# Kernel optimization log

Hardware: AMD Instinct MI355X
Metric: run time of the kernel (lower is better)

## Reference

```python
import jax, jax.numpy as jnp
import numpy as np


def setup_inputs() -> dict:
    key = jax.random.key(0)
    k1, k2, k3, k4, k5 = jax.random.split(key, 5)
    B, D_IN, D_OUT = 8192, 4096, 4096
    inp = jax.random.normal(k1, (B, D_IN), dtype=jnp.float32)
    # dir_loc: kaiming-like init then row-normalized (as in __init__)
    dir_loc = jax.random.normal(k2, (D_OUT, D_IN), dtype=jnp.float32) * np.sqrt(2.0 / D_IN)
    dir_loc = dir_loc / jnp.sqrt(jnp.sum(dir_loc ** 2, axis=-1, keepdims=True))
    # raw (softplus-inverse) concentration parameter
    dir_conc_raw = jax.random.uniform(k3, (D_OUT,), dtype=jnp.float32) + 3.0
    # rad_layer = nn.Linear(in, out): default torch init ~ U(-1/sqrt(in), 1/sqrt(in))
    bound = 1.0 / np.sqrt(D_IN)
    rad_w = jax.random.uniform(k4, (D_OUT, D_IN), minval=-bound, maxval=bound, dtype=jnp.float32)
    rad_b = jax.random.uniform(k5, (D_OUT,), minval=-bound, maxval=bound, dtype=jnp.float32)
    bias = jnp.zeros((D_OUT,), dtype=jnp.float32)  # initialized uniform(0,0)
    return {"input": inp, "dir_loc": dir_loc, "dir_conc_raw": dir_conc_raw,
            "rad_w": rad_w, "rad_b": rad_b, "bias": bias}


def reference(input, dir_loc, dir_conc_raw, rad_w, rad_b, bias):
    # sample=False path: direction_sample = PowerSpherical(loc, kappa).mean
    #   = loc * kappa / (kappa + dim - 1), kappa = softplus(raw)
    d = dir_loc.shape[1]
    kappa = jax.nn.softplus(dir_conc_raw)                      # [O]
    direction = dir_loc * (kappa / (kappa + (d - 1)))[:, None]  # [O, I]
    # radius = softplus(Linear(input))
    radius = jax.nn.softplus(input @ rad_w.T + rad_b)          # [B, O]
    # (input.unsqueeze(1) * (direction * radius[..., None])).sum(-1) + bias
    # == (input @ direction.T) * radius + bias  (GEMM + elementwise scale)
    return (input @ direction.T) * radius + bias
```

## Files before the change

kernel.cpp:

```cpp
#include <hip/hip_runtime.h>
#include <hip/hip_bf16.h>
#include <math.h>


typedef __bf16 bf16x8 __attribute__((ext_vector_type(8)));
typedef float  f32x4  __attribute__((ext_vector_type(4)));
typedef unsigned short u16;
typedef u16   u16x4 __attribute__((ext_vector_type(4)));
typedef float f4    __attribute__((ext_vector_type(4)));

#define BDIM 8192
#define IDIM 4096
#define ODIM 4096
#define BM 256
#define BN 128
#define BK 32
#define NKT (IDIM/BK)

__device__ __forceinline__ u16 f2bf(float x){ __bf16 h=(__bf16)x; return __builtin_bit_cast(u16,h); }
__device__ __forceinline__ float bf2f(u16 u){ return (float)__builtin_bit_cast(__bf16,u); }

__global__ void k_scale(const float* __restrict__ raw, float* __restrict__ scale){
  int o = blockIdx.x*256 + threadIdx.x;
  if(o < ODIM){
    float x = raw[o];
    float k = (x > 20.f) ? x : log1pf(expf(x));
    scale[o] = k / (k + (float)(IDIM-1));
  }
}

__global__ void k_split(const f4* __restrict__ src, u16x4* __restrict__ hi,
                        u16x4* __restrict__ lo, int n4){
  int i = blockIdx.x*blockDim.x + threadIdx.x;
  int stride = gridDim.x*blockDim.x;
  for(; i<n4; i+=stride){
    f4 v = src[i];
    u16x4 h, l;
    #pragma unroll
    for(int j=0;j<4;++j){
      float x = v[j];
      u16 hb = f2bf(x);
      h[j] = hb;
      l[j] = f2bf(x - bf2f(hb));
    }
    hi[i]=h; lo[i]=l;
  }
}

__global__ void k_split_dir(const f4* __restrict__ src, const float* __restrict__ scale,
                            u16x4* __restrict__ hi, u16x4* __restrict__ lo, int n4){
  int i = blockIdx.x*blockDim.x + threadIdx.x;
  int stride = gridDim.x*blockDim.x;
  for(; i<n4; i+=stride){
    float s = scale[i>>10];
    f4 v = src[i];
    u16x4 h, l;
    #pragma unroll
    for(int j=0;j<4;++j){
      float x = v[j]*s;
      u16 hb = f2bf(x);
      h[j] = hb;
      l[j] = f2bf(x - bf2f(hb));
    }
    hi[i]=h; lo[i]=l;
  }
}

__device__ __forceinline__ void async16(const u16* g, u16* l){
  __builtin_amdgcn_global_load_lds((const __attribute__((address_space(1))) void*)g,
                                   (__attribute__((address_space(3))) void*)l, 16, 0, 0);
}

__global__ __launch_bounds__(512,2) void k_gemm(
    const u16* __restrict__ Ah, const u16* __restrict__ Al,
    const u16* __restrict__ Rh, const u16* __restrict__ Rl,
    const u16* __restrict__ Dh, const u16* __restrict__ Dl,
    const float* __restrict__ rad_b, const float* __restrict__ bias,
    float* __restrict__ out)
{
  __shared__ __align__(16) u16 smem[2*32768];

  const int tid  = threadIdx.x;
  const int lane = tid & 63;
  const int wid  = tid >> 6;
  const int wr = wid >> 1, wc = wid & 1;

  const int bid = blockIdx.x;
  const int swz = (bid & 7)*128 + (bid >> 3);
  const int bm = swz >> 5;
  const int bn = swz & 31;

  const int r0   = tid >> 2;
  const int cxor = (r0 >> 1) & 3;
  const int c0   = ((tid & 3) ^ cxor) * 8;
  const size_t arow = (size_t)(bm*BM + r0)*IDIM + c0;
  const size_t brow = (size_t)(bn*BN + r0)*IDIM + c0;
  const u16* gAh = Ah + arow;  const u16* gAl = Al + arow;
  const u16* gRh = Rh + brow;  const u16* gRl = Rl + brow;
  const u16* gDh = Dh + brow;  const u16* gDl = Dl + brow;
  u16* dst = smem + tid*8;

  const int lr   = lane & 15;
  const int koff = (((lane >> 4) ^ ((lr >> 1) & 3))) * 8;
  const int aoff = (wr*64 + lr)*BK + koff;
  const int boff = (wc*64 + lr)*BK + koff;

  f32x4 accR[4][4] = {};
  f32x4 accD[4][4] = {};

#define MFMA16(A,B,C) __builtin_amdgcn_mfma_f32_16x16x32_bf16(A,B,C,0,0,0)

#define STAGE_FULL(BUF, KT) { \
    const int _k = (KT)*BK; \
    u16* _df = dst + (BUF)*32768; \
    async16(gAh + _k,            _df);         \
    async16(gAh + 128*IDIM + _k, _df + 4096);  \
    async16(gAl + _k,            _df + 8192);  \
    async16(gAl + 128*IDIM + _k, _df + 12288); \
    async16(gRh + _k,            _df + 16384); \
    async16(gRl + _k,            _df + 20480); \
    async16(gDh + _k,            _df + 24576); \
    async16(gDl + _k,            _df + 28672); \
  }

#define PH_PRE  __builtin_amdgcn_s_barrier(); \
    asm volatile("s_waitcnt lgkmcnt(0)" ::: "memory"); \
    __builtin_amdgcn_sched_barrier(0); \
    __builtin_amdgcn_s_setprio(1);
#define PH_POST __builtin_amdgcn_s_setprio(0); \
    __builtin_amdgcn_s_barrier(); \
    __builtin_amdgcn_sched_barrier(0);

#define K_TILE(BUF, VM, DOSTAGE, NEXTK) { \
    const u16* sb = smem + (BUF)*32768; \
    const int _ko = (NEXTK)*BK; \
    u16* _d = dst + (BUF)*32768; \
    bf16x8 ah[4], al[4]; \
    {  \
      bf16x8 b0[2], b1[2]; \
      _Pragma("unroll") for(int mi=0;mi<4;++mi){ \
        ah[mi] = *(const bf16x8*)(sb +        aoff + mi*512); \
        al[mi] = *(const bf16x8*)(sb + 8192 + aoff + mi*512); } \
      _Pragma("unroll") for(int ni=0;ni<2;++ni){ \
        b0[ni] = *(const bf16x8*)(sb + 16384 + boff + ni*512); \
        b1[ni] = *(const bf16x8*)(sb + 20480 + boff + ni*512); } \
      PH_PRE \
      _Pragma("unroll") for(int mi=0;mi<4;++mi) \
        _Pragma("unroll") for(int ni=0;ni<2;++ni){ \
          accR[mi][ni] = MFMA16(ah[mi], b0[ni], accR[mi][ni]); \
          accR[mi][ni] = MFMA16(ah[mi], b1[ni], accR[mi][ni]); \
          accR[mi][ni] = MFMA16(al[mi], b0[ni], accR[mi][ni]); } \
      PH_POST \
    } \
    {  \
      bf16x8 b0[2], b1[2]; \
      _Pragma("unroll") for(int ni=0;ni<2;++ni){ \
        b0[ni] = *(const bf16x8*)(sb + 16384 + boff + (ni+2)*512); \
        b1[ni] = *(const bf16x8*)(sb + 20480 + boff + (ni+2)*512); } \
      if (DOSTAGE) { \
        async16(gAh + _ko,            _d);         \
        async16(gAh + 128*IDIM + _ko, _d + 4096);  \
        async16(gAl + _ko,            _d + 8192);  \
        async16(gAl + 128*IDIM + _ko, _d + 12288); } \
      PH_PRE \
      _Pragma("unroll") for(int mi=0;mi<4;++mi) \
        _Pragma("unroll") for(int ni=0;ni<2;++ni){ \
          accR[mi][ni+2] = MFMA16(ah[mi], b0[ni], accR[mi][ni+2]); \
          accR[mi][ni+2] = MFMA16(ah[mi], b1[ni], accR[mi][ni+2]); \
          accR[mi][ni+2] = MFMA16(al[mi], b0[ni], accR[mi][ni+2]); } \
      PH_POST \
    } \
    {  \
      bf16x8 b0[2], b1[2]; \
      _Pragma("unroll") for(int ni=0;ni<2;++ni){ \
        b0[ni] = *(const bf16x8*)(sb + 24576 + boff + ni*512); \
        b1[ni] = *(const bf16x8*)(sb + 28672 + boff + ni*512); } \
      if (DOSTAGE) { \
        async16(gRh + _ko, _d + 16384); \
        async16(gRl + _ko, _d + 20480); } \
      PH_PRE \
      _Pragma("unroll") for(int mi=0;mi<4;++mi) \
        _Pragma("unroll") for(int ni=0;ni<2;++ni){ \
          accD[mi][ni] = MFMA16(ah[mi], b0[ni], accD[mi][ni]); \
          accD[mi][ni] = MFMA16(ah[mi], b1[ni], accD[mi][ni]); \
          accD[mi][ni] = MFMA16(al[mi], b0[ni], accD[mi][ni]); } \
      PH_POST \
    } \
    {  \
      bf16x8 b0[2], b1[2]; \
      _Pragma("unroll") for(int ni=0;ni<2;++ni){ \
        b0[ni] = *(const bf16x8*)(sb + 24576 + boff + (ni+2)*512); \
        b1[ni] = *(const bf16x8*)(sb + 28672 + boff + (ni+2)*512); } \
      PH_PRE \
      _Pragma("unroll") for(int mi=0;mi<4;++mi) \
        _Pragma("unroll") for(int ni=0;ni<2;++ni){ \
          accD[mi][ni+2] = MFMA16(ah[mi], b0[ni], accD[mi][ni+2]); \
          accD[mi][ni+2] = MFMA16(ah[mi], b1[ni], accD[mi][ni+2]); \
          accD[mi][ni+2] = MFMA16(al[mi], b0[ni], accD[mi][ni+2]); } \
      __builtin_amdgcn_s_setprio(0); \
      asm volatile("s_waitcnt vmcnt(" VM ")" ::: "memory"); \
      __builtin_amdgcn_s_barrier(); \
      __builtin_amdgcn_sched_barrier(0); \
      if (DOSTAGE) { \
        async16(gDh + _ko, _d + 24576); \
        async16(gDl + _ko, _d + 28672); } \
    } \
  }

  STAGE_FULL(0, 0)
  STAGE_FULL(1, 1)
  asm volatile("s_waitcnt vmcnt(8)" ::: "memory");
  __builtin_amdgcn_s_barrier();
  __builtin_amdgcn_sched_barrier(0);

  #pragma unroll 1
  for(int t=0; t<NKT-2; t+=2){
    K_TILE(0, "6", true, t+2)
    K_TILE(1, "6", true, t+3)
  }
  K_TILE(0, "0", false, 0)
  K_TILE(1, "0", false, 0)

#undef K_TILE
#undef PH_PRE
#undef PH_POST
#undef STAGE_FULL
#undef MFMA16

  const int orow0 = bm*BM + wr*64 + (lane>>4)*4;
  const int ocol0 = bn*BN + wc*64 + (lane & 15);
  #pragma unroll
  for(int ni=0;ni<4;++ni){
    const int col = ocol0 + ni*16;
    const float rb = rad_b[col];
    const float bs = bias[col];
    #pragma unroll
    for(int mi=0;mi<4;++mi){
      const int row = orow0 + mi*16;
      #pragma unroll
      for(int j=0;j<4;++j){
        float s  = accR[mi][ni][j] + rb;
        float sp = (s > 20.f) ? s : log1pf(expf(s));
        out[(size_t)(row+j)*ODIM + col] = accD[mi][ni][j]*sp + bs;
      }
    }
  }
}

extern "C" void kernel_launch(void* const* d_in, const int* in_sizes, int n_in,
                              void* d_out, int out_size, void* d_ws, size_t ws_size,
                              hipStream_t stream){
  (void)in_sizes; (void)n_in; (void)out_size; (void)ws_size;
  const float* inp  = (const float*)d_in[0];
  const float* dirl = (const float*)d_in[1];
  const float* draw = (const float*)d_in[2];
  const float* radw = (const float*)d_in[3];
  const float* radb = (const float*)d_in[4];
  const float* bias = (const float*)d_in[5];
  float* out = (float*)d_out;

  char* ws = (char*)d_ws;
  u16* Ah = (u16*)(ws);
  u16* Al = (u16*)(ws +  67108864L);
  u16* Rh = (u16*)(ws + 134217728L);
  u16* Rl = (u16*)(ws + 167772160L);
  u16* Dh = (u16*)(ws + 201326592L);
  u16* Dl = (u16*)(ws + 234881024L);
  float* scale = (float*)(ws + 268435456L);

  k_scale<<<dim3(ODIM/256), dim3(256), 0, stream>>>(draw, scale);

  const int n4A = BDIM*IDIM/4;
  const int n4W = ODIM*IDIM/4;
  k_split<<<dim3(2048), dim3(256), 0, stream>>>((const f4*)inp,  (u16x4*)Ah, (u16x4*)Al, n4A);
  k_split<<<dim3(2048), dim3(256), 0, stream>>>((const f4*)radw, (u16x4*)Rh, (u16x4*)Rl, n4W);
  k_split_dir<<<dim3(2048), dim3(256), 0, stream>>>((const f4*)dirl, scale, (u16x4*)Dh, (u16x4*)Dl, n4W);

  k_gemm<<<dim3((BDIM/BM)*(ODIM/BN)), dim3(512), 0, stream>>>(
      Ah, Al, Rh, Rl, Dh, Dl, radb, bias, out);
}
```

Baseline: 1.815 ms.

## Prefetch next k-tile A and R fragments from LDS across phases in GEMM loop

Restructures the k-tile loop so A-high/low and the first R fragments for the next tile are read from the other LDS buffer during the current tile's later phases. The reads are ping-ponged through register sets xah/yah. Waits become partial lgkmcnt counts instead of full drains. The goal is to hide LDS read latency behind MFMA work and shorten the stall at each phase barrier. In exchange it raises register pressure, which can cost occupancy or cause spills, and it makes the vmcnt and barrier ordering harder to keep correct.

```diff
diff --git a/kernel.cpp b/kernel.cpp
--- a/kernel.cpp
+++ b/kernel.cpp
@@ -108,6 +108,8 @@
   f32x4 accR[4][4] = {};
   f32x4 accD[4][4] = {};
 
+  bf16x8 xah[4], xal[4], yah[4], yal[4], rbh[2], rbl[2];
+
 #define MFMA16(A,B,C) __builtin_amdgcn_mfma_f32_16x16x32_bf16(A,B,C,0,0,0)
 
 #define STAGE_FULL(BUF, KT) { \
@@ -123,88 +125,91 @@
     async16(gDl + _k,            _df + 28672); \
   }
 
-#define PH_PRE  __builtin_amdgcn_s_barrier(); \
-    asm volatile("s_waitcnt lgkmcnt(0)" ::: "memory"); \
+#define PH_PRE(J) \
+    __builtin_amdgcn_sched_barrier(0); \
+    __builtin_amdgcn_s_barrier(); \
+    asm volatile("s_waitcnt lgkmcnt(" J ")" ::: "memory"); \
     __builtin_amdgcn_sched_barrier(0); \
     __builtin_amdgcn_s_setprio(1);
-#define PH_POST __builtin_amdgcn_s_setprio(0); \
+#define PH_POST \
+    __builtin_amdgcn_s_setprio(0); \
     __builtin_amdgcn_s_barrier(); \
     __builtin_amdgcn_sched_barrier(0);
-
-#define K_TILE(BUF, VM, DOSTAGE, NEXTK) { \
+#define PH_POST_VM(VM) \
+    __builtin_amdgcn_s_setprio(0); \
+    asm volatile("s_waitcnt vmcnt(" VM ")" ::: "memory"); \
+    __builtin_amdgcn_s_barrier(); \
+    __builtin_amdgcn_sched_barrier(0);
+
+#define K_TILE(BUF, CAH,CAL, NAH,NAL, VM1, VM2, DOSTAGE, NEXTK) { \
     const u16* sb = smem + (BUF)*32768; \
+    const u16* nb = smem + ((BUF)^1)*32768; \
+    u16* _d = dst + (BUF)*32768; \
     const int _ko = (NEXTK)*BK; \
-    u16* _d = dst + (BUF)*32768; \
-    bf16x8 ah[4], al[4]; \
-    {  \
-      bf16x8 b0[2], b1[2]; \
-      _Pragma("unroll") for(int mi=0;mi<4;++mi){ \
-        ah[mi] = *(const bf16x8*)(sb +        aoff + mi*512); \
-        al[mi] = *(const bf16x8*)(sb + 8192 + aoff + mi*512); } \
-      _Pragma("unroll") for(int ni=0;ni<2;++ni){ \
-        b0[ni] = *(const bf16x8*)(sb + 16384 + boff + ni*512); \
-        b1[ni] = *(const bf16x8*)(sb + 20480 + boff + ni*512); } \
-      PH_PRE \
-      _Pragma("unroll") for(int mi=0;mi<4;++mi) \
-        _Pragma("unroll") for(int ni=0;ni<2;++ni){ \
-          accR[mi][ni] = MFMA16(ah[mi], b0[ni], accR[mi][ni]); \
-          accR[mi][ni] = MFMA16(ah[mi], b1[ni], accR[mi][ni]); \
-          accR[mi][ni] = MFMA16(al[mi], b0[ni], accR[mi][ni]); } \
-      PH_POST \
-    } \
-    {  \
-      bf16x8 b0[2], b1[2]; \
-      _Pragma("unroll") for(int ni=0;ni<2;++ni){ \
-        b0[ni] = *(const bf16x8*)(sb + 16384 + boff + (ni+2)*512); \
-        b1[ni] = *(const bf16x8*)(sb + 20480 + boff + (ni+2)*512); } \
-      if (DOSTAGE) { \
-        async16(gAh + _ko,            _d);         \
-        async16(gAh + 128*IDIM + _ko, _d + 4096);  \
-        async16(gAl + _ko,            _d + 8192);  \
-        async16(gAl + 128*IDIM + _ko, _d + 12288); } \
-      PH_PRE \
-      _Pragma("unroll") for(int mi=0;mi<4;++mi) \
-        _Pragma("unroll") for(int ni=0;ni<2;++ni){ \
-          accR[mi][ni+2] = MFMA16(ah[mi], b0[ni], accR[mi][ni+2]); \
-          accR[mi][ni+2] = MFMA16(ah[mi], b1[ni], accR[mi][ni+2]); \
-          accR[mi][ni+2] = MFMA16(al[mi], b0[ni], accR[mi][ni+2]); } \
-      PH_POST \
-    } \
-    {  \
-      bf16x8 b0[2], b1[2]; \
-      _Pragma("unroll") for(int ni=0;ni<2;++ni){ \
-        b0[ni] = *(const bf16x8*)(sb + 24576 + boff + ni*512); \
-        b1[ni] = *(const bf16x8*)(sb + 28672 + boff + ni*512); } \
-      if (DOSTAGE) { \
-        async16(gRh + _ko, _d + 16384); \
-        async16(gRl + _ko, _d + 20480); } \
-      PH_PRE \
-      _Pragma("unroll") for(int mi=0;mi<4;++mi) \
-        _Pragma("unroll") for(int ni=0;ni<2;++ni){ \
-          accD[mi][ni] = MFMA16(ah[mi], b0[ni], accD[mi][ni]); \
-          accD[mi][ni] = MFMA16(ah[mi], b1[ni], accD[mi][ni]); \
-          accD[mi][ni] = MFMA16(al[mi], b0[ni], accD[mi][ni]); } \
-      PH_POST \
-    } \
-    {  \
-      bf16x8 b0[2], b1[2]; \
-      _Pragma("unroll") for(int ni=0;ni<2;++ni){ \
-        b0[ni] = *(const bf16x8*)(sb + 24576 + boff + (ni+2)*512); \
-        b1[ni] = *(const bf16x8*)(sb + 28672 + boff + (ni+2)*512); } \
-      PH_PRE \
-      _Pragma("unroll") for(int mi=0;mi<4;++mi) \
-        _Pragma("unroll") for(int ni=0;ni<2;++ni){ \
-          accD[mi][ni+2] = MFMA16(ah[mi], b0[ni], accD[mi][ni+2]); \
-          accD[mi][ni+2] = MFMA16(ah[mi], b1[ni], accD[mi][ni+2]); \
-          accD[mi][ni+2] = MFMA16(al[mi], b0[ni], accD[mi][ni+2]); } \
-      __builtin_amdgcn_s_setprio(0); \
-      asm volatile("s_waitcnt vmcnt(" VM ")" ::: "memory"); \
-      __builtin_amdgcn_s_barrier(); \
-      __builtin_amdgcn_sched_barrier(0); \
-      if (DOSTAGE) { \
-        async16(gDh + _ko, _d + 24576); \
-        async16(gDl + _ko, _d + 28672); } \
-    } \
+    bf16x8 bh2[2], bl2[2], dh1[2], dl1[2], dh2[2], dl2[2]; \
+     \
+    _Pragma("unroll") for(int ni=0;ni<2;++ni){ \
+      bh2[ni] = *(const bf16x8*)(sb + 16384 + boff + (2+ni)*512); \
+      bl2[ni] = *(const bf16x8*)(sb + 20480 + boff + (2+ni)*512); } \
+    PH_PRE("4") \
+    _Pragma("unroll") for(int mi=0;mi<4;++mi) \
+      _Pragma("unroll") for(int ni=0;ni<2;++ni){ \
+        accR[mi][ni] = MFMA16(CAH[mi], rbh[ni], accR[mi][ni]); \
+        accR[mi][ni] = MFMA16(CAH[mi], rbl[ni], accR[mi][ni]); \
+        accR[mi][ni] = MFMA16(CAL[mi], rbh[ni], accR[mi][ni]); } \
+    PH_POST \
+     \
+     \
+    if (DOSTAGE) { \
+      async16(gAh + _ko,            _d);         \
+      async16(gAh + 128*IDIM + _ko, _d + 4096);  \
+      async16(gAl + _ko,            _d + 8192);  \
+      async16(gAl + 128*IDIM + _ko, _d + 12288); } \
+    _Pragma("unroll") for(int ni=0;ni<2;++ni){ \
+      dh1[ni] = *(const bf16x8*)(sb + 24576 + boff + ni*512); \
+      dl1[ni] = *(const bf16x8*)(sb + 28672 + boff + ni*512); } \
+    PH_PRE("4") \
+    _Pragma("unroll") for(int mi=0;mi<4;++mi) \
+      _Pragma("unroll") for(int ni=0;ni<2;++ni){ \
+        accR[mi][2+ni] = MFMA16(CAH[mi], bh2[ni], accR[mi][2+ni]); \
+        accR[mi][2+ni] = MFMA16(CAH[mi], bl2[ni], accR[mi][2+ni]); \
+        accR[mi][2+ni] = MFMA16(CAL[mi], bh2[ni], accR[mi][2+ni]); } \
+    PH_POST_VM(VM1)  \
+     \
+     \
+    if (DOSTAGE) { \
+      async16(gRh + _ko, _d + 16384); \
+      async16(gRl + _ko, _d + 20480); } \
+    _Pragma("unroll") for(int ni=0;ni<2;++ni){ \
+      dh2[ni] = *(const bf16x8*)(sb + 24576 + boff + (2+ni)*512); \
+      dl2[ni] = *(const bf16x8*)(sb + 28672 + boff + (2+ni)*512); } \
+    _Pragma("unroll") for(int mi=0;mi<4;++mi) \
+      NAH[mi] = *(const bf16x8*)(nb + aoff + mi*512); \
+    PH_PRE("8") \
+    _Pragma("unroll") for(int mi=0;mi<4;++mi) \
+      _Pragma("unroll") for(int ni=0;ni<2;++ni){ \
+        accD[mi][ni] = MFMA16(CAH[mi], dh1[ni], accD[mi][ni]); \
+        accD[mi][ni] = MFMA16(CAH[mi], dl1[ni], accD[mi][ni]); \
+        accD[mi][ni] = MFMA16(CAL[mi], dh1[ni], accD[mi][ni]); } \
+    PH_POST \
+     \
+     \
+    _Pragma("unroll") for(int mi=0;mi<4;++mi) \
+      NAL[mi] = *(const bf16x8*)(nb + 8192 + aoff + mi*512); \
+    _Pragma("unroll") for(int ni=0;ni<2;++ni){ \
+      rbh[ni] = *(const bf16x8*)(nb + 16384 + boff + ni*512); \
+      rbl[ni] = *(const bf16x8*)(nb + 20480 + boff + ni*512); } \
+    PH_PRE("8") \
+    _Pragma("unroll") for(int mi=0;mi<4;++mi) \
+      _Pragma("unroll") for(int ni=0;ni<2;++ni){ \
+        accD[mi][2+ni] = MFMA16(CAH[mi], dh2[ni], accD[mi][2+ni]); \
+        accD[mi][2+ni] = MFMA16(CAH[mi], dl2[ni], accD[mi][2+ni]); \
+        accD[mi][2+ni] = MFMA16(CAL[mi], dh2[ni], accD[mi][2+ni]); } \
+    PH_POST_VM(VM2)  \
+    if (DOSTAGE) { \
+      async16(gDh + _ko, _d + 24576); \
+      async16(gDl + _ko, _d + 28672); } \
+    __builtin_amdgcn_sched_barrier(0); \
   }
 
   STAGE_FULL(0, 0)
@@ -212,18 +217,30 @@
   asm volatile("s_waitcnt vmcnt(8)" ::: "memory");
   __builtin_amdgcn_s_barrier();
   __builtin_amdgcn_sched_barrier(0);
+  #pragma unroll
+  for(int mi=0;mi<4;++mi){
+    xah[mi] = *(const bf16x8*)(smem +        aoff + mi*512);
+    xal[mi] = *(const bf16x8*)(smem + 8192 + aoff + mi*512);
+  }
+  #pragma unroll
+  for(int ni=0;ni<2;++ni){
+    rbh[ni] = *(const bf16x8*)(smem + 16384 + boff + ni*512);
+    rbl[ni] = *(const bf16x8*)(smem + 20480 + boff + ni*512);
+  }
+  __builtin_amdgcn_sched_barrier(0);
 
   #pragma unroll 1
   for(int t=0; t<NKT-2; t+=2){
-    K_TILE(0, "6", true, t+2)
-    K_TILE(1, "6", true, t+3)
-  }
-  K_TILE(0, "0", false, 0)
-  K_TILE(1, "0", false, 0)
+    K_TILE(0, xah,xal, yah,yal, "6","6", 1, t+2)
+    K_TILE(1, yah,yal, xah,xal, "6","6", 1, t+3)
+  }
+  K_TILE(0, xah,xal, yah,yal, "2","0", 0, 0)
+  K_TILE(1, yah,yal, xah,xal, "0","0", 0, 0)
 
 #undef K_TILE
 #undef PH_PRE
 #undef PH_POST
+#undef PH_POST_VM
 #undef STAGE_FULL
 #undef MFMA16
 
```

After: 2.012 ms. 10.9% more time.
